# Kernel optimization log

Hardware: AMD Instinct MI355X
Metric: run time of the kernel (lower is better)

The kernel has to match this reference:

```python
import jax, jax.numpy as jnp
import numpy as np

B, C, HI, WI = 16, 256, 64, 64
DT = 512
NH = 8
EPS = 1e-5

def setup_inputs():
    key = jax.random.key(0)
    ks = jax.random.split(key, 16)
    def w(k, shape):
        return jax.random.normal(k, shape, jnp.float32) * 0.02
    return {
        'F_vis': jax.random.normal(ks[0], (B, C, HI, WI), jnp.float32),
        'F_text': jax.random.normal(ks[1], (B, DT), jnp.float32),
        'F_unified': jax.random.normal(ks[2], (B, DT), jnp.float32),
        'F_teacher': jax.random.normal(ks[3], (B, DT), jnp.float32),
        'tp_w1': w(ks[4], (DT, C)), 'tp_b1': jnp.zeros((C,), jnp.float32),
        'tp_w2': w(ks[5], (C, C)), 'tp_b2': jnp.zeros((C,), jnp.float32),
        'q_w': w(ks[6], (C, C)), 'q_b': jnp.zeros((C,), jnp.float32),
        'k_w': w(ks[7], (C, C)), 'k_b': jnp.zeros((C,), jnp.float32),
        'v_w': w(ks[8], (C, C)), 'v_b': jnp.zeros((C,), jnp.float32),
        'o_w': w(ks[9], (C, C)), 'o_b': jnp.zeros((C,), jnp.float32),
        'fa_w': w(ks[10], (DT, 1)), 'fa_b': jnp.zeros((1,), jnp.float32),
        'gp_w': w(ks[11], (DT, C)), 'gp_b': jnp.zeros((C,), jnp.float32),
        'ln_g': jnp.ones((C,), jnp.float32), 'ln_b': jnp.zeros((C,), jnp.float32),
    }

def reference(F_vis, F_text, F_unified, F_teacher, tp_w1, tp_b1, tp_w2, tp_b2, q_w, q_b, k_w, k_b, v_w, v_b, o_w, o_b, fa_w, fa_b, gp_w, gp_b, ln_g, ln_b):
    b, c, h, w_ = F_vis.shape
    T = h * w_
    hd = c // NH
    x = F_vis.reshape(b, c, T).transpose(0, 2, 1)  # [B,T,C] vision tokens
    # text projection -> single query (T_q = 1)
    t = jax.nn.gelu(F_text @ tp_w1 + tp_b1, approximate=False) @ tp_w2 + tp_b2  # [B,C]
    q = (t @ q_w + q_b).reshape(b, NH, hd)                       # [B,H,hd]
    kh = (x @ k_w + k_b).reshape(b, T, NH, hd)                   # [B,T,H,hd]
    vh = (x @ v_w + v_b).reshape(b, T, NH, hd)
    scores = jnp.einsum('bhd,bthd->bht', q, kh) * (hd ** -0.5)   # [B,H,T]
    attn = jax.nn.softmax(scores, axis=-1)                        # dropout = identity at eval
    z = jnp.einsum('bht,bthd->bhd', attn, vh).reshape(b, c)      # [B,C]
    z = z @ o_w + o_b                                             # out_proj once; expand is a broadcast of identical rows
    # student-teacher joint gate
    f_stack = jnp.stack([F_unified, F_teacher], axis=1)           # [B,2,DT]
    a = jax.nn.softmax(f_stack @ fa_w + fa_b, axis=1)             # [B,2,1]
    f_cond = jnp.sum(a * f_stack, axis=1)                         # [B,DT]
    g = jax.nn.sigmoid(f_cond @ gp_w + gp_b)                      # [B,C]
    # residual + gated fusion + LayerNorm over channel dim
    y = x + g[:, None, :] * z[:, None, :]                         # [B,T,C]
    mu = jnp.mean(y, axis=-1, keepdims=True)
    var = jnp.var(y, axis=-1, keepdims=True)
    y = (y - mu) * jax.lax.rsqrt(var + EPS) * ln_g + ln_b
    out = y.transpose(0, 2, 1).reshape(b, c, h, w_)
    return out, attn[:, :, None, :]  # attn_weights [B,H,1,T] as in torch
```

## Files before the change

kernel.cpp:

```cpp
#include <hip/hip_runtime.h>
#include <math.h>

#define B_  16
#define C_  256
#define T_  4096
#define DT_ 512
#define NH_ 8
#define HD_ 32

__global__ __launch_bounds__(512) void k_t1gate(
    const float* __restrict__ F_text, const float* __restrict__ U,
    const float* __restrict__ Tt,
    const float* __restrict__ tp_w1, const float* __restrict__ tp_b1,
    const float* __restrict__ fa_w,  const float* __restrict__ fa_b,
    const float* __restrict__ gp_w,  const float* __restrict__ gp_b,
    float* __restrict__ t1, float* __restrict__ gout)
{
    __shared__ float xs[8192];
    __shared__ float part[8192];
    __shared__ float pd[2][16][32];
    __shared__ float a0s[16], a1s[16];
    int tid = threadIdx.x;
    int c0  = blockIdx.x * 16;
    int cl  = tid & 15, ks = tid >> 4;
    int c   = c0 + cl;

    for (int idx = tid; idx < 8192; idx += 512) xs[idx] = F_text[idx];
    __syncthreads();
    {
        float acc[16];
        #pragma unroll
        for (int b = 0; b < 16; ++b) acc[b] = 0.f;
        const float* wp = tp_w1 + (size_t)(ks * 16) * 256 + c;
        #pragma unroll
        for (int i = 0; i < 16; ++i) {
            float w = wp[(size_t)i * 256];
            int xi = ks * 16 + i;
            #pragma unroll
            for (int b = 0; b < 16; ++b) acc[b] += xs[b * 512 + xi] * w;
        }
        #pragma unroll
        for (int b = 0; b < 16; ++b) part[ks * 256 + b * 16 + cl] = acc[b];
    }
    __syncthreads();
    if (tid < 256) {
        int b = tid >> 4, cc = tid & 15;
        float s = 0.f;
        #pragma unroll
        for (int k2 = 0; k2 < 32; ++k2) s += part[k2 * 256 + b * 16 + cc];
        s += tp_b1[c0 + cc];
        s = 0.5f * s * (1.0f + erff(s * 0.70710678118654752f));
        t1[b * 256 + c0 + cc] = s;
    }
    __syncthreads();

    {
        int b = tid >> 5, sl = tid & 31;
        const float* ub = U  + b * 512 + sl * 16;
        const float* tb = Tt + b * 512 + sl * 16;
        const float* fw = fa_w + sl * 16;
        float su = 0.f, st = 0.f;
        #pragma unroll
        for (int j = 0; j < 16; ++j) { su += ub[j] * fw[j]; st += tb[j] * fw[j]; }
        pd[0][b][sl] = su; pd[1][b][sl] = st;
    }
    __syncthreads();
    if (tid < 16) {
        float s0 = fa_b[0], s1 = fa_b[0];
        #pragma unroll
        for (int sl = 0; sl < 32; ++sl) { s0 += pd[0][tid][sl]; s1 += pd[1][tid][sl]; }
        float mm = fmaxf(s0, s1);
        float e0 = expf(s0 - mm), e1 = expf(s1 - mm);
        float inv = 1.0f / (e0 + e1);
        a0s[tid] = e0 * inv; a1s[tid] = e1 * inv;
    }
    __syncthreads();
    for (int idx = tid; idx < 8192; idx += 512) {
        int b = idx >> 9;
        xs[idx] = a0s[b] * U[idx] + a1s[b] * Tt[idx];
    }
    __syncthreads();
    {
        float acc[16];
        #pragma unroll
        for (int b = 0; b < 16; ++b) acc[b] = 0.f;
        const float* wp = gp_w + (size_t)(ks * 16) * 256 + c;
        #pragma unroll
        for (int i = 0; i < 16; ++i) {
            float w = wp[(size_t)i * 256];
            int xi = ks * 16 + i;
            #pragma unroll
            for (int b = 0; b < 16; ++b) acc[b] += xs[b * 512 + xi] * w;
        }
        #pragma unroll
        for (int b = 0; b < 16; ++b) part[ks * 256 + b * 16 + cl] = acc[b];
    }
    __syncthreads();
    if (tid < 256) {
        int b = tid >> 4, cc = tid & 15;
        float s = 0.f;
        #pragma unroll
        for (int k2 = 0; k2 < 32; ++k2) s += part[k2 * 256 + b * 16 + cc];
        s += gp_b[c0 + cc];
        gout[b * 256 + c0 + cc] = 1.0f / (1.0f + expf(-s));
    }
}

template<int K, int ACT>
__global__ __launch_bounds__(512) void gemm16(const float* __restrict__ x,
                                              const float* __restrict__ W,
                                              const float* __restrict__ bias,
                                              float* __restrict__ out)
{
    __shared__ float xs[16 * K];
    __shared__ float part[32 * 256];
    int tid = threadIdx.x;
    int c0  = blockIdx.x * 16;

    for (int idx = tid; idx < 16 * K; idx += 512) xs[idx] = x[idx];
    __syncthreads();

    int cl = tid & 15, ks = tid >> 4;
    const int Kc = K / 32;
    int c = c0 + cl;

    float acc[16];
    #pragma unroll
    for (int b = 0; b < 16; ++b) acc[b] = 0.f;

    const float* wp = W + (size_t)(ks * Kc) * 256 + c;
    #pragma unroll
    for (int i = 0; i < Kc; ++i) {
        float w  = wp[(size_t)i * 256];
        int   xi = ks * Kc + i;
        #pragma unroll
        for (int b = 0; b < 16; ++b) acc[b] += xs[b * K + xi] * w;
    }
    #pragma unroll
    for (int b = 0; b < 16; ++b) part[ks * 256 + b * 16 + cl] = acc[b];
    __syncthreads();

    if (tid < 256) {
        int b = tid >> 4, cc = tid & 15;
        float s = 0.f;
        #pragma unroll
        for (int k2 = 0; k2 < 32; ++k2) s += part[k2 * 256 + b * 16 + cc];
        s += bias[c0 + cc];
        if (ACT == 1) s = 0.5f * s * (1.0f + erff(s * 0.70710678118654752f));
        out[b * 256 + c0 + cc] = s;
    }
}

__global__ __launch_bounds__(512) void k_qkq(const float* __restrict__ tv,
                                             const float* __restrict__ q_w,
                                             const float* __restrict__ q_b,
                                             const float* __restrict__ k_w,
                                             const float* __restrict__ k_b,
                                             float* __restrict__ kq,
                                             float* __restrict__ qkb)
{
    __shared__ float xs[4096];
    __shared__ float part[8192];
    __shared__ float qs[512];
    int tid = threadIdx.x;
    int h   = blockIdx.x;

    for (int idx = tid; idx < 4096; idx += 512) xs[idx] = tv[idx];
    __syncthreads();

    {
        int cl = tid & 31, ks = tid >> 5;
        float acc[16];
        #pragma unroll
        for (int b = 0; b < 16; ++b) acc[b] = 0.f;
        const float* wp = q_w + (size_t)(ks * 16) * 256 + h * HD_ + cl;
        #pragma unroll
        for (int i = 0; i < 16; ++i) {
            float w = wp[(size_t)i * 256];
            int xi = ks * 16 + i;
            #pragma unroll
            for (int b = 0; b < 16; ++b) acc[b] += xs[b * 256 + xi] * w;
        }
        #pragma unroll
        for (int b = 0; b < 16; ++b) part[(ks * 16 + b) * 32 + cl] = acc[b];
    }
    __syncthreads();
    {
        int b = tid >> 5, cl = tid & 31;
        float s = 0.f;
        #pragma unroll
        for (int k2 = 0; k2 < 16; ++k2) s += part[(k2 * 16 + b) * 32 + cl];
        qs[b * 32 + cl] = s + q_b[h * HD_ + cl];
    }
    __syncthreads();
    if (tid < 16) {
        float s = 0.f;
        #pragma unroll
        for (int d = 0; d < 32; ++d) s += qs[tid * 32 + d] * k_b[h * HD_ + d];
        qkb[tid * NH_ + h] = s;
    }

    {
        int c = tid >> 1, bh = tid & 1;
        const float4* kwp = reinterpret_cast<const float4*>(k_w + (size_t)c * 256 + h * HD_);
        float4 kw[8];
        #pragma unroll
        for (int j = 0; j < 8; ++j) kw[j] = kwp[j];
        float acc[8] = {0,0,0,0,0,0,0,0};
        #pragma unroll
        for (int j = 0; j < 8; ++j) {
            float w0 = kw[j].x, w1 = kw[j].y, w2 = kw[j].z, w3 = kw[j].w;
            #pragma unroll
            for (int bi = 0; bi < 8; ++bi) {
                const float* qp = &qs[(bh * 8 + bi) * 32 + j * 4];
                acc[bi] += qp[0] * w0 + qp[1] * w1 + qp[2] * w2 + qp[3] * w3;
            }
        }
        #pragma unroll
        for (int bi = 0; bi < 8; ++bi)
            kq[((size_t)((bh * 8 + bi) * NH_ + h)) * C_ + c] = acc[bi];
    }
}

__global__ __launch_bounds__(512) void k2_scores(const float* __restrict__ F_vis,
                                                 const float* __restrict__ kq,
                                                 const float* __restrict__ qkb,
                                                 float* __restrict__ e,
                                                 float* __restrict__ ms,
                                                 float* __restrict__ xac)
{
    int tc = blockIdx.x;
    int b  = blockIdx.y;
    int tid = threadIdx.x;
    int t0 = tc * 256;
    const float scale = 0.176776695296636893f;

    __shared__ float kqs[256][9];
    __shared__ __align__(16) float4 part4[8 * 8 * 64];
    __shared__ __align__(16) float esf[8 * 256];
    __shared__ float qkbs[8];
    __shared__ float redm[8][4], reds[8][4];

    for (int idx = tid; idx < 2048; idx += 512) {
        int c = idx & 255, h = idx >> 8;
        kqs[c][h] = kq[((size_t)(b * NH_ + h)) * C_ + c];
    }
    if (tid < 8) qkbs[tid] = qkb[b * NH_ + tid];
    __syncthreads();

    {
        int cs = tid >> 6, t4 = tid & 63;
        const float* fv = F_vis + ((size_t)b * C_) * T_ + t0 + t4 * 4;
        float4 acc[8];
        #pragma unroll
        for (int h = 0; h < 8; ++h) acc[h] = make_float4(0.f, 0.f, 0.f, 0.f);
        #pragma unroll 8
        for (int i = 0; i < 32; ++i) {
            int c = i * 8 + cs;
            float4 v = *reinterpret_cast<const float4*>(&fv[(size_t)c * T_]);
            #pragma unroll
            for (int h = 0; h < 8; ++h) {
                float w = kqs[c][h];
                acc[h].x += v.x * w; acc[h].y += v.y * w;
                acc[h].z += v.z * w; acc[h].w += v.w * w;
            }
        }
        #pragma unroll
        for (int h = 0; h < 8; ++h) part4[(cs * 8 + h) * 64 + t4] = acc[h];
    }
    __syncthreads();

    {
        int tl = tid & 255, hg = tid >> 8;
        int lane = tid & 63, wid = tid >> 6;
        const float* pf = reinterpret_cast<const float*>(part4);
        float sv[4], mh[4];
        #pragma unroll
        for (int hh = 0; hh < 4; ++hh) {
            int h = hg * 4 + hh;
            float s = 0.f;
            #pragma unroll
            for (int cs = 0; cs < 8; ++cs) s += pf[(cs * 8 + h) * 256 + tl];
            sv[hh] = (s + qkbs[h]) * scale;
            float m = sv[hh];
            #pragma unroll
            for (int o = 32; o; o >>= 1) m = fmaxf(m, __shfl_xor(m, o));
            mh[hh] = m;
        }
        if (lane == 0) {
            #pragma unroll
            for (int hh = 0; hh < 4; ++hh) redm[hg * 4 + hh][wid & 3] = mh[hh];
        }
        __syncthreads();
        float ev[4];
        #pragma unroll
        for (int hh = 0; hh < 4; ++hh) {
            int h = hg * 4 + hh;
            float m = fmaxf(fmaxf(redm[h][0], redm[h][1]), fmaxf(redm[h][2], redm[h][3]));
            ev[hh] = expf(sv[hh] - m);
            e[((size_t)(b * NH_ + h)) * T_ + t0 + tl] = ev[hh];
            esf[h * 256 + tl] = ev[hh];
            float sm = ev[hh];
            #pragma unroll
            for (int o = 32; o; o >>= 1) sm += __shfl_xor(sm, o);
            if (lane == 0) reds[h][wid & 3] = sm;
        }
        __syncthreads();
        if (tid < 8) {
            float m = fmaxf(fmaxf(redm[tid][0], redm[tid][1]),
                            fmaxf(redm[tid][2], redm[tid][3]));
            float sum = reds[tid][0] + reds[tid][1] + reds[tid][2] + reds[tid][3];
            size_t base = (((size_t)(b * NH_ + tid)) * 16 + tc) * 2;
            ms[base]     = m;
            ms[base + 1] = sum;
        }
    }

    {
        int lane = tid & 63, wid = tid >> 6;
        int cl = lane & 15, tq = lane >> 4;
        const float4* es4 = reinterpret_cast<const float4*>(esf);
        #pragma unroll
        for (int pass = 0; pass < 2; ++pass) {
            int c = pass * 128 + wid * 16 + cl;
            const float* fvc = F_vis + ((size_t)b * C_ + c) * T_ + t0;
            float p[8] = {0, 0, 0, 0, 0, 0, 0, 0};
            #pragma unroll 4
            for (int i = 0; i < 16; ++i) {
                int Q = tq * 16 + i;
                float4 v = *reinterpret_cast<const float4*>(&fvc[Q * 4]);
                #pragma unroll
                for (int h = 0; h < 8; ++h) {
                    float4 E = es4[h * 64 + Q];
                    p[h] += v.x * E.x + v.y * E.y + v.z * E.z + v.w * E.w;
                }
            }
            #pragma unroll
            for (int h = 0; h < 8; ++h) {
                p[h] += __shfl_xor(p[h], 16);
                p[h] += __shfl_xor(p[h], 32);
            }
            if (tq == 0) {
                #pragma unroll
                for (int h = 0; h < 8; ++h)
                    xac[(((size_t)tc * B_ + b) * NH_ + h) * C_ + c] = p[h];
            }
        }
    }
}

__global__ __launch_bounds__(256) void k5_merge(const float* __restrict__ e,
                                               const float* __restrict__ ms,
                                               const float* __restrict__ xac,
                                               const float* __restrict__ v_w,
                                               const float* __restrict__ v_b,
                                               const float* __restrict__ o_w,
                                               const float* __restrict__ o_b,
                                               const float* __restrict__ g,
                                               float* __restrict__ attn,
                                               float* __restrict__ gz)
{
    int b = blockIdx.x, tid = threadIdx.x;
    __shared__ float fact[8][16];
    __shared__ float xaL[8][256];
    __shared__ float zp[256];
    __shared__ float Ms[8], iZs[8];

    if (tid < 8) {
        const float* mp = ms + ((size_t)(b * NH_ + tid)) * 32;
        float M = -1e30f;
        #pragma unroll
        for (int ck = 0; ck < 16; ++ck) M = fmaxf(M, mp[ck * 2]);
        float Z = 0.f;
        #pragma unroll
        for (int ck = 0; ck < 16; ++ck) Z += mp[ck * 2 + 1] * expf(mp[ck * 2] - M);
        Ms[tid] = M; iZs[tid] = 1.0f / Z;
    }
    __syncthreads();
    if (tid < 128) {
        int h = tid >> 4, ck = tid & 15;
        fact[h][ck] = expf(ms[((size_t)(b * NH_ + h)) * 32 + ck * 2] - Ms[h]) * iZs[h];
    }
    __syncthreads();

    const float4* eb = reinterpret_cast<const float4*>(e + (size_t)b * NH_ * T_);
    float4* ab = reinterpret_cast<float4*>(attn + (size_t)b * NH_ * T_);
    for (int idx = tid; idx < NH_ * T_ / 4; idx += 256) {
        int h  = idx >> 10;
        int tq = idx & 1023;
        float f = fact[h][tq >> 6];
        float4 a = eb[idx];
        a.x *= f; a.y *= f; a.z *= f; a.w *= f;
        ab[idx] = a;
    }

    for (int idx = tid; idx < 2048; idx += 256) {
        int h = idx >> 8, c = idx & 255;
        float s = 0.f;
        #pragma unroll
        for (int ck = 0; ck < 16; ++ck)
            s += xac[(((size_t)ck * B_ + b) * NH_ + h) * C_ + c] * fact[h][ck];
        xaL[h][c] = s;
    }
    __syncthreads();

    {
        int h = tid >> 5;
        float s = v_b[tid];
        #pragma unroll 8
        for (int c = 0; c < 256; ++c) s += xaL[h][c] * v_w[c * 256 + tid];
        zp[tid] = s;
    }
    __syncthreads();
    {
        float z = o_b[tid];
        #pragma unroll 8
        for (int i = 0; i < 256; ++i) z += zp[i] * o_w[i * 256 + tid];
        gz[b * 256 + tid] = g[b * 256 + tid] * z;
    }
}

__global__ __launch_bounds__(256) void k6_ln(const float* __restrict__ F_vis,
                                             const float* __restrict__ gz,
                                             const float* __restrict__ ln_g,
                                             const float* __restrict__ ln_b,
                                             float* __restrict__ out)
{
    int b  = blockIdx.y;
    int t0 = blockIdx.x * 32;
    int tid = threadIdx.x;
    int t4 = tid & 7;
    int cb = tid >> 3;

    __shared__ float gzs[256], lgs[256], lbs[256];
    __shared__ float4 redS[4][8], redQ[4][8];
    __shared__ float4 mu4s[8], rs4s[8];

    gzs[tid] = gz[b * C_ + tid];
    lgs[tid] = ln_g[tid];
    lbs[tid] = ln_b[tid];
    __syncthreads();

    const float* fvb = F_vis + (size_t)b * C_ * T_ + t0 + t4 * 4;
    float4 v[8];
    float4 s = make_float4(0.f, 0.f, 0.f, 0.f);
    float4 q = make_float4(0.f, 0.f, 0.f, 0.f);
    #pragma unroll
    for (int k = 0; k < 8; ++k) {
        int c = cb + k * 32;
        float4 x = *reinterpret_cast<const float4*>(&fvb[(size_t)c * T_]);
        float gc = gzs[c];
        x.x += gc; x.y += gc; x.z += gc; x.w += gc;
        v[k] = x;
        s.x += x.x; s.y += x.y; s.z += x.z; s.w += x.w;
        q.x += x.x * x.x; q.y += x.y * x.y; q.z += x.z * x.z; q.w += x.w * x.w;
    }
    #pragma unroll
    for (int o = 8; o <= 32; o <<= 1) {
        s.x += __shfl_xor(s.x, o); s.y += __shfl_xor(s.y, o);
        s.z += __shfl_xor(s.z, o); s.w += __shfl_xor(s.w, o);
        q.x += __shfl_xor(q.x, o); q.y += __shfl_xor(q.y, o);
        q.z += __shfl_xor(q.z, o); q.w += __shfl_xor(q.w, o);
    }
    int wid = tid >> 6;
    if ((tid & 63) < 8) { redS[wid][t4] = s; redQ[wid][t4] = q; }
    __syncthreads();
    if (tid < 8) {
        float4 S = redS[0][tid], Q = redQ[0][tid];
        #pragma unroll
        for (int w = 1; w < 4; ++w) {
            float4 a = redS[w][tid], c2 = redQ[w][tid];
            S.x += a.x; S.y += a.y; S.z += a.z; S.w += a.w;
            Q.x += c2.x; Q.y += c2.y; Q.z += c2.z; Q.w += c2.w;
        }
        float4 mu, rs;
        mu.x = S.x * (1.0f / C_); mu.y = S.y * (1.0f / C_);
        mu.z = S.z * (1.0f / C_); mu.w = S.w * (1.0f / C_);
        rs.x = rsqrtf(fmaxf(Q.x * (1.0f / C_) - mu.x * mu.x, 0.f) + 1e-5f);
        rs.y = rsqrtf(fmaxf(Q.y * (1.0f / C_) - mu.y * mu.y, 0.f) + 1e-5f);
        rs.z = rsqrtf(fmaxf(Q.z * (1.0f / C_) - mu.z * mu.z, 0.f) + 1e-5f);
        rs.w = rsqrtf(fmaxf(Q.w * (1.0f / C_) - mu.w * mu.w, 0.f) + 1e-5f);
        mu4s[tid] = mu; rs4s[tid] = rs;
    }
    __syncthreads();
    float4 mu = mu4s[t4], rs = rs4s[t4];
    float* ob = out + (size_t)b * C_ * T_ + t0 + t4 * 4;
    #pragma unroll
    for (int k = 0; k < 8; ++k) {
        int c = cb + k * 32;
        float lg = lgs[c], lb = lbs[c];
        float4 o;
        o.x = (v[k].x - mu.x) * rs.x * lg + lb;
        o.y = (v[k].y - mu.y) * rs.y * lg + lb;
        o.z = (v[k].z - mu.z) * rs.z * lg + lb;
        o.w = (v[k].w - mu.w) * rs.w * lg + lb;
        *reinterpret_cast<float4*>(&ob[(size_t)c * T_]) = o;
    }
}

extern "C" void kernel_launch(void* const* d_in, const int* in_sizes, int n_in,
                              void* d_out, int out_size, void* d_ws, size_t ws_size,
                              hipStream_t stream)
{
    const float* F_vis     = (const float*)d_in[0];
    const float* F_text    = (const float*)d_in[1];
    const float* F_unified = (const float*)d_in[2];
    const float* F_teacher = (const float*)d_in[3];
    const float* tp_w1 = (const float*)d_in[4];
    const float* tp_b1 = (const float*)d_in[5];
    const float* tp_w2 = (const float*)d_in[6];
    const float* tp_b2 = (const float*)d_in[7];
    const float* q_w   = (const float*)d_in[8];
    const float* q_b   = (const float*)d_in[9];
    const float* k_w   = (const float*)d_in[10];
    const float* k_b   = (const float*)d_in[11];
    const float* v_w   = (const float*)d_in[12];
    const float* v_b   = (const float*)d_in[13];
    const float* o_w   = (const float*)d_in[14];
    const float* o_b   = (const float*)d_in[15];
    const float* fa_w  = (const float*)d_in[16];
    const float* fa_b  = (const float*)d_in[17];
    const float* gp_w  = (const float*)d_in[18];
    const float* gp_b  = (const float*)d_in[19];
    const float* ln_g  = (const float*)d_in[20];
    const float* ln_b  = (const float*)d_in[21];

    float* ws  = (float*)d_ws;
    float* t1  = ws;
    float* tv  = ws + 4096;
    float* kq  = ws + 8192;
    float* qkb = ws + 40960;
    float* g   = ws + 41088;
    float* gz  = ws + 45184;
    float* e   = ws + 49280;
    float* ms  = ws + 573568;
    float* xac = ws + 577664;

    float* out  = (float*)d_out;
    float* attn = out + (size_t)B_ * C_ * T_;

    k_t1gate<<<16, 512, 0, stream>>>(F_text, F_unified, F_teacher,
                                     tp_w1, tp_b1, fa_w, fa_b, gp_w, gp_b,
                                     t1, g);
    gemm16<256, 0><<<16, 512, 0, stream>>>(t1, tp_w2, tp_b2, tv);
    k_qkq<<<NH_, 512, 0, stream>>>(tv, q_w, q_b, k_w, k_b, kq, qkb);

    k2_scores<<<dim3(16, B_), 512, 0, stream>>>(F_vis, kq, qkb, e, ms, xac);
    k5_merge<<<B_, 256, 0, stream>>>(e, ms, xac, v_w, v_b, o_w, o_b, g, attn, gz);
    k6_ln<<<dim3(128, B_), 256, 0, stream>>>(F_vis, gz, ln_g, ln_b, out);
}
```

Measured before the change: 105.4 us.

## Split merge kernel into parallel attn rescale and split-K gz projection

The old merge kernel ran only 16 blocks of 256 threads and did the attention-weight rescale, the V projection and the O projection serially inside each block. The attn rescale now runs in its own kernel over a 16x16 grid, so the 2 MB normalized-attention write is spread across many CUs. The V and O projections now use 1024-thread blocks with a four-way split-K and a shared-memory reduction. The change adds one kernel launch, and the gz path is still limited to 16 blocks.

```diff
diff --git a/kernel.cpp b/kernel.cpp
--- a/kernel.cpp
+++ b/kernel.cpp
@@ -349,20 +349,50 @@
     }
 }
 
-__global__ __launch_bounds__(256) void k5_merge(const float* __restrict__ e,
-                                               const float* __restrict__ ms,
+__global__ __launch_bounds__(256) void k5a_attn(const float* __restrict__ e,
+                                                const float* __restrict__ ms,
+                                                float* __restrict__ attn)
+{
+    int tc = blockIdx.x, b = blockIdx.y, tid = threadIdx.x;
+    __shared__ float facts[8];
+    if (tid < 8) {
+        const float* mp = ms + ((size_t)(b * NH_ + tid)) * 32;
+        float M = -1e30f;
+        #pragma unroll
+        for (int ck = 0; ck < 16; ++ck) M = fmaxf(M, mp[ck * 2]);
+        float Z = 0.f;
+        #pragma unroll
+        for (int ck = 0; ck < 16; ++ck) Z += mp[ck * 2 + 1] * expf(mp[ck * 2] - M);
+        facts[tid] = expf(mp[tc * 2] - M) / Z;
+    }
+    __syncthreads();
+    #pragma unroll
+    for (int idx = tid; idx < 512; idx += 256) {
+        int h = idx >> 6, tq = idx & 63;
+        const float4* ep = reinterpret_cast<const float4*>(
+            e + ((size_t)(b * NH_ + h)) * T_ + tc * 256);
+        float4* ap = reinterpret_cast<float4*>(
+            attn + ((size_t)(b * NH_ + h)) * T_ + tc * 256);
+        float f = facts[h];
+        float4 a = ep[tq];
+        a.x *= f; a.y *= f; a.z *= f; a.w *= f;
+        ap[tq] = a;
+    }
+}
+
+__global__ __launch_bounds__(1024) void k5b_gz(const float* __restrict__ ms,
                                                const float* __restrict__ xac,
                                                const float* __restrict__ v_w,
                                                const float* __restrict__ v_b,
                                                const float* __restrict__ o_w,
                                                const float* __restrict__ o_b,
                                                const float* __restrict__ g,
-                                               float* __restrict__ attn,
                                                float* __restrict__ gz)
 {
     int b = blockIdx.x, tid = threadIdx.x;
     __shared__ float fact[8][16];
-    __shared__ float xaL[8][256];
+    __shared__ float xaL[2048];
+    __shared__ float part[4][256];
     __shared__ float zp[256];
     __shared__ float Ms[8], iZs[8];
 
@@ -383,39 +413,38 @@
     }
     __syncthreads();
 
-    const float4* eb = reinterpret_cast<const float4*>(e + (size_t)b * NH_ * T_);
-    float4* ab = reinterpret_cast<float4*>(attn + (size_t)b * NH_ * T_);
-    for (int idx = tid; idx < NH_ * T_ / 4; idx += 256) {
-        int h  = idx >> 10;
-        int tq = idx & 1023;
-        float f = fact[h][tq >> 6];
-        float4 a = eb[idx];
-        a.x *= f; a.y *= f; a.z *= f; a.w *= f;
-        ab[idx] = a;
-    }
-
-    for (int idx = tid; idx < 2048; idx += 256) {
+    for (int idx = tid; idx < 2048; idx += 1024) {
         int h = idx >> 8, c = idx & 255;
         float s = 0.f;
         #pragma unroll
         for (int ck = 0; ck < 16; ++ck)
             s += xac[(((size_t)ck * B_ + b) * NH_ + h) * C_ + c] * fact[h][ck];
-        xaL[h][c] = s;
-    }
-    __syncthreads();
-
-    {
-        int h = tid >> 5;
-        float s = v_b[tid];
+        xaL[idx] = s;
+    }
+    __syncthreads();
+
+    {
+        int j = tid & 255, ks = tid >> 8;
+        int h = j >> 5;
+        float s = 0.f;
         #pragma unroll 8
-        for (int c = 0; c < 256; ++c) s += xaL[h][c] * v_w[c * 256 + tid];
-        zp[tid] = s;
-    }
-    __syncthreads();
-    {
-        float z = o_b[tid];
+        for (int c = ks * 64; c < ks * 64 + 64; ++c) s += xaL[h * 256 + c] * v_w[c * 256 + j];
+        part[ks][j] = s;
+    }
+    __syncthreads();
+    if (tid < 256)
+        zp[tid] = part[0][tid] + part[1][tid] + part[2][tid] + part[3][tid] + v_b[tid];
+    __syncthreads();
+    {
+        int j = tid & 255, ks = tid >> 8;
+        float s = 0.f;
         #pragma unroll 8
-        for (int i = 0; i < 256; ++i) z += zp[i] * o_w[i * 256 + tid];
+        for (int i = ks * 64; i < ks * 64 + 64; ++i) s += zp[i] * o_w[i * 256 + j];
+        part[ks][j] = s;
+    }
+    __syncthreads();
+    if (tid < 256) {
+        float z = part[0][tid] + part[1][tid] + part[2][tid] + part[3][tid] + o_b[tid];
         gz[b * 256 + tid] = g[b * 256 + tid] * z;
     }
 }
@@ -546,6 +575,7 @@
     k_qkq<<<NH_, 512, 0, stream>>>(tv, q_w, q_b, k_w, k_b, kq, qkb);
 
     k2_scores<<<dim3(16, B_), 512, 0, stream>>>(F_vis, kq, qkb, e, ms, xac);
-    k5_merge<<<B_, 256, 0, stream>>>(e, ms, xac, v_w, v_b, o_w, o_b, g, attn, gz);
+    k5a_attn<<<dim3(16, B_), 256, 0, stream>>>(e, ms, attn);
+    k5b_gz<<<B_, 1024, 0, stream>>>(ms, xac, v_w, v_b, o_w, o_b, g, gz);
     k6_ln<<<dim3(128, B_), 256, 0, stream>>>(F_vis, gz, ln_g, ln_b, out);
 }
```

Result: faster. 88.68 us (-15.9%).
